# Kernel tuning notes

Measured on AMD Instinct MI355X. Metric: run time of the kernel, lower is better.

The kernel has to match this reference:

```python
import jax, jax.numpy as jnp
import numpy as np

L, ND, ED, AD = 2, 128, 64, 64
N, E, A, G = 50000, 300000, 600000, 16
EPS = 1e-5


def _graph_norm(h, batch, num_graphs, w, b):
    # PyG LayerNorm(mode='graph'): scalar mean/var over all nodes*features per graph.
    F = h.shape[-1]
    cnt = jax.ops.segment_sum(jnp.ones(h.shape[0], h.dtype), batch, num_segments=num_graphs)
    norm = jnp.maximum(cnt, 1.0) * F  # [G]
    mean = (jax.ops.segment_sum(h, batch, num_segments=num_graphs).sum(-1) / norm)[batch][:, None]
    hc = h - mean
    var = (jax.ops.segment_sum(hc * hc, batch, num_segments=num_graphs).sum(-1) / norm)
    out = hc * jax.lax.rsqrt(var + EPS)[batch][:, None]
    return out * w + b


def setup_inputs() -> dict:
    key = jax.random.key(0)
    ks = jax.random.split(key, 24)

    def lin(k, fi, fo):
        return jax.random.normal(k, (L, fi, fo), jnp.float32) / jnp.sqrt(float(fi))

    inp = {
        "x": jax.random.normal(ks[0], (N, ND), jnp.float32),
        "edge_attr": jax.random.normal(ks[1], (E, ED), jnp.float32),
        "angle_attr": jax.random.normal(ks[2], (A, AD), jnp.float32),
        # node_edge_mlp: [2*ND+ED -> ED], plain linear (plain_last=True)
        "W_ne": lin(ks[3], 2 * ND + ED, ED), "b_ne": jnp.zeros((L, ED), jnp.float32),
        "g_e": jnp.ones((L, ED), jnp.float32), "be_e": jnp.zeros((L, ED), jnp.float32),
        # edge_angle_mlp: [2*ED+AD -> AD]
        "W_ea": lin(ks[4], 2 * ED + AD, AD), "b_ea": jnp.zeros((L, AD), jnp.float32),
        "g_a": jnp.ones((L, AD), jnp.float32), "be_a": jnp.zeros((L, AD), jnp.float32),
        # edge_graph_mp message net: [2*ED+AD -> ED]
        "W_emp": lin(ks[5], 2 * ED + AD, ED), "b_emp": jnp.zeros((L, ED), jnp.float32),
        "g_emp": jnp.ones((L, ED), jnp.float32), "be_emp": jnp.zeros((L, ED), jnp.float32),
        # node_graph_mp message net: [2*ND+ED -> ND]
        "W_nmp": lin(ks[6], 2 * ND + ED, ND), "b_nmp": jnp.zeros((L, ND), jnp.float32),
        "g_nmp": jnp.ones((L, ND), jnp.float32), "be_nmp": jnp.zeros((L, ND), jnp.float32),
        "node_batch": jnp.sort(jax.random.randint(ks[7], (N,), 0, G)),
        "edge_index": jax.random.randint(ks[8], (2, E), 0, N),
        "edge_batch": jnp.sort(jax.random.randint(ks[9], (E,), 0, G)),
        "threebody_index": jax.random.randint(ks[10], (2, A), 0, E),
        "angle_batch": jnp.sort(jax.random.randint(ks[11], (A,), 0, G)),
        "num_graphs": G,
    }
    return inp


def reference(x, edge_attr, angle_attr,
              W_ne, b_ne, g_e, be_e,
              W_ea, b_ea, g_a, be_a,
              W_emp, b_emp, g_emp, be_emp,
              W_nmp, b_nmp, g_nmp, be_nmp,
              node_batch, edge_index, edge_batch,
              threebody_index, angle_batch, num_graphs):
    src_e, dst_e = edge_index[0], edge_index[1]
    src_t, dst_t = threebody_index[0], threebody_index[1]
    n_nodes, n_edges = x.shape[0], edge_attr.shape[0]
    for i in range(W_ne.shape[0]):
        # node-pair -> edge update + residual + graph norm
        ecat = jnp.concatenate([x[src_e], x[dst_e], edge_attr], axis=-1)
        edge_attr = edge_attr + ecat @ W_ne[i] + b_ne[i]
        edge_attr = _graph_norm(edge_attr, edge_batch, num_graphs, g_e[i], be_e[i])
        # edge-pair -> angle update + residual + graph norm
        acat = jnp.concatenate([edge_attr[src_t], edge_attr[dst_t], angle_attr], axis=-1)
        angle_attr = angle_attr + acat @ W_ea[i] + b_ea[i]
        angle_attr = _graph_norm(angle_attr, angle_batch, num_graphs, g_a[i], be_a[i])
        # edge_graph_mp: angle-mediated message passing over edges
        mcat = jnp.concatenate([edge_attr[src_t], edge_attr[dst_t], angle_attr], axis=-1)
        msg = jax.nn.relu(mcat @ W_emp[i] + b_emp[i])
        agg = jax.ops.segment_sum(msg, dst_t, num_segments=n_edges)
        edge_attr = _graph_norm(edge_attr + agg, edge_batch, num_graphs, g_emp[i], be_emp[i])
        # node_graph_mp: edge-mediated message passing over nodes
        ncat = jnp.concatenate([x[src_e], x[dst_e], edge_attr], axis=-1)
        nmsg = jax.nn.relu(ncat @ W_nmp[i] + b_nmp[i])
        nagg = jax.ops.segment_sum(nmsg, dst_e, num_segments=n_nodes)
        x = _graph_norm(x + nagg, node_batch, num_graphs, g_nmp[i], be_nmp[i])
    return x
```

## Files before the change

### kernel.cpp

```cpp
#include <hip/hip_runtime.h>

typedef __attribute__((ext_vector_type(8))) short bf16x8_t;
typedef __attribute__((ext_vector_type(4))) short bf16x4_t;
typedef __attribute__((ext_vector_type(4))) float f32x4_t;

constexpr int NG = 16;
constexpr float EPS = 1e-5f;

__device__ inline unsigned short f2bf(float f) {
  unsigned u = __builtin_bit_cast(unsigned, f);
  u += 0x7FFFu + ((u >> 16) & 1u);
  return (unsigned short)(u >> 16);
}
__device__ inline float bf2f(unsigned short u) {
  unsigned x = ((unsigned)u) << 16;
  return __builtin_bit_cast(float, x);
}

template<bool F32>
__device__ inline void ldrow8(const void* base, size_t off, float v[8]) {
  if constexpr (F32) {
    const float* p = (const float*)base + off;
    float4 f0 = *(const float4*)p, f1 = *(const float4*)(p + 4);
    v[0]=f0.x; v[1]=f0.y; v[2]=f0.z; v[3]=f0.w;
    v[4]=f1.x; v[5]=f1.y; v[6]=f1.z; v[7]=f1.w;
  } else {
    bf16x8_t t = *(const bf16x8_t*)((const unsigned short*)base + off);
#pragma unroll
    for (int k = 0; k < 8; ++k) v[k] = bf2f((unsigned short)t[k]);
  }
}

__global__ __launch_bounds__(256) void k_dense_x(
    const float* __restrict__ x,
    const unsigned short* __restrict__ WtNE,
    const unsigned short* __restrict__ WtNM,
    unsigned short* __restrict__ P, int nN)
{
  int gw = (int)((blockIdx.x * 256u + threadIdx.x) >> 6);
  int ntile = nN >> 4;
  if (gw >= ntile) return;
  int lane = threadIdx.x & 63;
  int colb = lane & 15;
  int ko = (lane >> 4) << 3;
  int rowb = (lane >> 4) << 2;
  int row = (gw << 4) + colb;
  const float* xr = x + (size_t)row * 128;
  f32x4_t a1[4] = {}, a2[4] = {}, a3[8] = {}, a4[8] = {};
#pragma unroll
  for (int c = 0; c < 4; ++c) {
    float4 f0 = *(const float4*)(xr + c * 32 + ko);
    float4 f1 = *(const float4*)(xr + c * 32 + ko + 4);
    float vv[8] = {f0.x,f0.y,f0.z,f0.w,f1.x,f1.y,f1.z,f1.w};
    bf16x8_t a;
#pragma unroll
    for (int k = 0; k < 8; ++k) a[k] = (short)f2bf(vv[k]);
#pragma unroll
    for (int nb = 0; nb < 4; ++nb) {
      bf16x8_t b1 = *(const bf16x8_t*)(WtNE + (size_t)(nb * 16 + colb) * 320 + c * 32 + ko);
      a1[nb] = __builtin_amdgcn_mfma_f32_16x16x32_bf16(a, b1, a1[nb], 0, 0, 0);
      bf16x8_t b2 = *(const bf16x8_t*)(WtNE + (size_t)(nb * 16 + colb) * 320 + (c + 4) * 32 + ko);
      a2[nb] = __builtin_amdgcn_mfma_f32_16x16x32_bf16(a, b2, a2[nb], 0, 0, 0);
    }
#pragma unroll
    for (int nb = 0; nb < 8; ++nb) {
      bf16x8_t b3 = *(const bf16x8_t*)(WtNM + (size_t)(nb * 16 + colb) * 320 + c * 32 + ko);
      a3[nb] = __builtin_amdgcn_mfma_f32_16x16x32_bf16(a, b3, a3[nb], 0, 0, 0);
      bf16x8_t b4 = *(const bf16x8_t*)(WtNM + (size_t)(nb * 16 + colb) * 320 + (c + 4) * 32 + ko);
      a4[nb] = __builtin_amdgcn_mfma_f32_16x16x32_bf16(a, b4, a4[nb], 0, 0, 0);
    }
  }
#pragma unroll
  for (int r = 0; r < 4; ++r) {
    size_t ro = (size_t)((gw << 4) + rowb + r) * 384;
    bf16x4_t t1, t2;
#pragma unroll
    for (int nb = 0; nb < 4; ++nb) { t1[nb] = (short)f2bf(a1[nb][r]); t2[nb] = (short)f2bf(a2[nb][r]); }
    *(bf16x4_t*)(P + ro + colb * 4) = t1;
    *(bf16x4_t*)(P + ro + 64 + colb * 4) = t2;
    bf16x8_t t3, t4;
#pragma unroll
    for (int nb = 0; nb < 8; ++nb) { t3[nb] = (short)f2bf(a3[nb][r]); t4[nb] = (short)f2bf(a4[nb][r]); }
    *(bf16x8_t*)(P + ro + 128 + colb * 8) = t3;
    *(bf16x8_t*)(P + ro + 256 + colb * 8) = t4;
  }
}

__global__ __launch_bounds__(256) void k_prep_e(
    const unsigned short* __restrict__ eA, const int* __restrict__ ebatch,
    const float* __restrict__ afA, const float* __restrict__ afB,
    const unsigned short* __restrict__ WtA,
    const unsigned short* __restrict__ WtP,
    unsigned short* __restrict__ PAE, int nE)
{
  __shared__ float lA[1024], lB[1024];
  for (int i = threadIdx.x; i < 1024; i += 256) { lA[i] = afA[i]; lB[i] = afB[i]; }
  __syncthreads();
  int gw = (int)((blockIdx.x * 256u + threadIdx.x) >> 6);
  int ntile = nE >> 4;
  if (gw >= ntile) return;
  int lane = threadIdx.x & 63;
  int colb = lane & 15;
  int ko = (lane >> 4) << 3;
  int rowb = (lane >> 4) << 2;
  int row = (gw << 4) + colb;
  int ge = ebatch[row];
  f32x4_t pa1[4] = {}, pa2[4] = {}, pe3[4] = {}, pe4[4] = {};
#pragma unroll
  for (int c2 = 0; c2 < 2; ++c2) {
    int fb = c2 * 32 + ko;
    bf16x8_t t = *(const bf16x8_t*)(eA + (size_t)row * 64 + fb);
    bf16x8_t an;
#pragma unroll
    for (int k = 0; k < 8; ++k)
      an[k] = (short)f2bf(bf2f((unsigned short)t[k]) * lA[ge*64 + fb + k] + lB[ge*64 + fb + k]);
#pragma unroll
    for (int nb = 0; nb < 4; ++nb) {
      size_t wb = (size_t)(nb * 16 + colb) * 192;
      bf16x8_t b;
      b = *(const bf16x8_t*)(WtA + wb + c2 * 32 + ko);
      pa1[nb] = __builtin_amdgcn_mfma_f32_16x16x32_bf16(an, b, pa1[nb], 0, 0, 0);
      b = *(const bf16x8_t*)(WtA + wb + 64 + c2 * 32 + ko);
      pa2[nb] = __builtin_amdgcn_mfma_f32_16x16x32_bf16(an, b, pa2[nb], 0, 0, 0);
      b = *(const bf16x8_t*)(WtP + wb + c2 * 32 + ko);
      pe3[nb] = __builtin_amdgcn_mfma_f32_16x16x32_bf16(an, b, pe3[nb], 0, 0, 0);
      b = *(const bf16x8_t*)(WtP + wb + 64 + c2 * 32 + ko);
      pe4[nb] = __builtin_amdgcn_mfma_f32_16x16x32_bf16(an, b, pe4[nb], 0, 0, 0);
    }
  }
#pragma unroll
  for (int r = 0; r < 4; ++r) {
    size_t ro = (size_t)((gw << 4) + rowb + r) * 256;
    bf16x8_t sH, dH;
#pragma unroll
    for (int nb = 0; nb < 4; ++nb) {
      sH[nb] = (short)f2bf(pa1[nb][r]); sH[4 + nb] = (short)f2bf(pe3[nb][r]);
      dH[nb] = (short)f2bf(pa2[nb][r]); dH[4 + nb] = (short)f2bf(pe4[nb][r]);
    }
    *(bf16x8_t*)(PAE + ro + colb * 8) = sH;
    *(bf16x8_t*)(PAE + ro + 128 + colb * 8) = dH;
  }
}

template<bool EF32>
__global__ __launch_bounds__(256) void k_edge(
    const unsigned short* __restrict__ P, const void* e_in, unsigned short* e_out,
    const int* __restrict__ ei, const int* __restrict__ ebatch,
    const unsigned short* __restrict__ Wt,
    const float* __restrict__ bias,
    const float* __restrict__ afA, const float* __restrict__ afB,
    float* __restrict__ gs1, float* __restrict__ gs2, int nE)
{
  __shared__ float lA[1024], lB[1024];
  __shared__ float ls1[NG], ls2[NG];
  __shared__ __align__(16) unsigned short tl[4][16][72];
  for (int i = threadIdx.x; i < 1024; i += 256) { lA[i] = afA[i]; lB[i] = afB[i]; }
  if (threadIdx.x < NG) { ls1[threadIdx.x] = 0.f; ls2[threadIdx.x] = 0.f; }
  __syncthreads();
  int gw = (int)((blockIdx.x * 256u + threadIdx.x) >> 6);
  int ntile = nE >> 4;
  bool act = gw < ntile;
  int lane = threadIdx.x & 63;
  int wid = threadIdx.x >> 6;
  int colb = lane & 15;
  int ko = (lane >> 4) << 3;
  int rowb = (lane >> 4) << 2;
  float sr[4] = {0.f,0.f,0.f,0.f}, ssr[4] = {0.f,0.f,0.f,0.f};
  if (act) {
    int sI[4], dI[4];
#pragma unroll
    for (int r = 0; r < 4; ++r) {
      int e_r = (gw << 4) + rowb + r;
      sI[r] = ei[e_r]; dI[r] = ei[nE + e_r];
    }
    bf16x4_t g1[4], g2[4];
#pragma unroll
    for (int r = 0; r < 4; ++r) {
      g1[r] = *(const bf16x4_t*)(P + (size_t)sI[r] * 384 + colb * 4);
      g2[r] = *(const bf16x4_t*)(P + (size_t)dI[r] * 384 + 64 + colb * 4);
    }
    int row = (gw << 4) + colb;
    int ge = ebatch[row];
    f32x4_t acc[4] = {};
#pragma unroll
    for (int c2 = 0; c2 < 2; ++c2) {
      int fb = c2 * 32 + ko;
      float vv[8];
      ldrow8<EF32>(e_in, (size_t)row * 64 + fb, vv);
      bf16x8_t a;
#pragma unroll
      for (int k = 0; k < 8; ++k) a[k] = (short)f2bf(vv[k] * lA[ge*64 + fb + k] + lB[ge*64 + fb + k]);
      *(bf16x8_t*)&tl[wid][colb][fb] = a;
#pragma unroll
      for (int nb = 0; nb < 4; ++nb) {
        bf16x8_t b = *(const bf16x8_t*)(Wt + (size_t)(nb * 16 + colb) * 320 + (8 + c2) * 32 + ko);
        acc[nb] = __builtin_amdgcn_mfma_f32_16x16x32_bf16(a, b, acc[nb], 0, 0, 0);
      }
    }
#pragma unroll
    for (int r = 0; r < 4; ++r) {
      int e_ = (gw << 4) + rowb + r;
#pragma unroll
      for (int nb = 0; nb < 4; ++nb) {
        int col = nb * 16 + colb;
        size_t off = (size_t)e_ * 64 + col;
        float nv = bf2f(tl[wid][rowb + r][col]);
        float vv = nv + bias[col]
                 + acc[nb][r] + bf2f((unsigned short)g1[r][nb]) + bf2f((unsigned short)g2[r][nb]);
        e_out[off] = f2bf(vv);
        sr[r] += vv; ssr[r] += vv * vv;
      }
    }
  }
#pragma unroll
  for (int m = 1; m <= 8; m <<= 1)
#pragma unroll
    for (int r = 0; r < 4; ++r) { sr[r] += __shfl_xor(sr[r], m); ssr[r] += __shfl_xor(ssr[r], m); }
  if (act && colb == 0) {
#pragma unroll
    for (int r = 0; r < 4; ++r) {
      int g = ebatch[(gw << 4) + rowb + r];
      atomicAdd(&ls1[g], sr[r]); atomicAdd(&ls2[g], ssr[r]);
    }
  }
  __syncthreads();
  if (threadIdx.x < NG) {
    atomicAdd(&gs1[threadIdx.x], ls1[threadIdx.x]);
    atomicAdd(&gs2[threadIdx.x], ls2[threadIdx.x]);
  }
}

template<bool AF32>
__global__ __launch_bounds__(256) void k_angle(
    const unsigned short* __restrict__ PAE,
    const void* a_in, unsigned short* a_out,
    const int* __restrict__ ti, const int* __restrict__ abatch,
    const unsigned short* __restrict__ Wt,
    const float* __restrict__ bias,
    const float* __restrict__ afAA, const float* __restrict__ afAB,
    float* __restrict__ gs1, float* __restrict__ gs2,
    unsigned short* __restrict__ pe, int nA)
{
  __shared__ float lAA[1024], lAB[1024];
  __shared__ float ls1[NG], ls2[NG];
  __shared__ __align__(16) unsigned short tl[4][16][72];
  for (int i = threadIdx.x; i < 1024; i += 256) { lAA[i] = afAA[i]; lAB[i] = afAB[i]; }
  if (threadIdx.x < NG) { ls1[threadIdx.x] = 0.f; ls2[threadIdx.x] = 0.f; }
  __syncthreads();
  int gw = (int)((blockIdx.x * 256u + threadIdx.x) >> 6);
  int ntile = nA >> 4;
  bool act = gw < ntile;
  int lane = threadIdx.x & 63;
  int wid = threadIdx.x >> 6;
  int colb = lane & 15;
  int ko = (lane >> 4) << 3;
  int rowb = (lane >> 4) << 2;
  float sr[4] = {0.f,0.f,0.f,0.f}, ssr[4] = {0.f,0.f,0.f,0.f};
  if (act) {
    int sI[4], dI[4];
#pragma unroll
    for (int r = 0; r < 4; ++r) {
      int a_r = (gw << 4) + rowb + r;
      sI[r] = ti[a_r]; dI[r] = ti[nA + a_r];
    }
    bf16x8_t gS[4], gD[4];
#pragma unroll
    for (int r = 0; r < 4; ++r) {
      gS[r] = *(const bf16x8_t*)(PAE + (size_t)sI[r] * 256 + colb * 8);
      gD[r] = *(const bf16x8_t*)(PAE + (size_t)dI[r] * 256 + 128 + colb * 8);
    }
    int row = (gw << 4) + colb;
    int ga = abatch[row];
    f32x4_t acc[4] = {};
#pragma unroll
    for (int c2 = 0; c2 < 2; ++c2) {
      int fb = c2 * 32 + ko;
      float vv[8];
      ldrow8<AF32>(a_in, (size_t)row * 64 + fb, vv);
      bf16x8_t a;
#pragma unroll
      for (int k = 0; k < 8; ++k) a[k] = (short)f2bf(vv[k] * lAA[ga*64 + fb + k] + lAB[ga*64 + fb + k]);
      *(bf16x8_t*)&tl[wid][colb][fb] = a;
#pragma unroll
      for (int nb = 0; nb < 4; ++nb) {
        bf16x8_t b = *(const bf16x8_t*)(Wt + (size_t)(nb * 16 + colb) * 192 + 128 + c2 * 32 + ko);
        acc[nb] = __builtin_amdgcn_mfma_f32_16x16x32_bf16(a, b, acc[nb], 0, 0, 0);
      }
    }
#pragma unroll
    for (int r = 0; r < 4; ++r) {
      int a_ = (gw << 4) + rowb + r;
#pragma unroll
      for (int nb = 0; nb < 4; ++nb) {
        int col = nb * 16 + colb;
        size_t off = (size_t)a_ * 64 + col;
        float nv = bf2f(tl[wid][rowb + r][col]);
        float vv = nv + bias[col] + acc[nb][r]
                 + bf2f((unsigned short)gS[r][nb]) + bf2f((unsigned short)gD[r][nb]);
        a_out[off] = f2bf(vv);
        sr[r] += vv; ssr[r] += vv * vv;
      }
      bf16x4_t pv;
#pragma unroll
      for (int nb = 0; nb < 4; ++nb)
        pv[nb] = (short)f2bf(bf2f((unsigned short)gS[r][4 + nb]) + bf2f((unsigned short)gD[r][4 + nb]));
      *(bf16x4_t*)(pe + (size_t)a_ * 64 + colb * 4) = pv;
    }
  }
#pragma unroll
  for (int m = 1; m <= 8; m <<= 1)
#pragma unroll
    for (int r = 0; r < 4; ++r) { sr[r] += __shfl_xor(sr[r], m); ssr[r] += __shfl_xor(ssr[r], m); }
  if (act && colb == 0) {
#pragma unroll
    for (int r = 0; r < 4; ++r) {
      int g = abatch[(gw << 4) + rowb + r];
      atomicAdd(&ls1[g], sr[r]); atomicAdd(&ls2[g], ssr[r]);
    }
  }
  __syncthreads();
  if (threadIdx.x < NG) {
    atomicAdd(&gs1[threadIdx.x], ls1[threadIdx.x]);
    atomicAdd(&gs2[threadIdx.x], ls2[threadIdx.x]);
  }
}

__global__ __launch_bounds__(256) void k_fin_emp(
    const unsigned short* __restrict__ a_, const int* __restrict__ abatch,
    const unsigned short* __restrict__ Wt,
    const float* __restrict__ bias,
    const float* __restrict__ afAA, const float* __restrict__ afAB,
    unsigned short* __restrict__ msg, int nA)
{
  __shared__ float lAA[1024], lAB[1024];
  for (int i = threadIdx.x; i < 1024; i += 256) { lAA[i] = afAA[i]; lAB[i] = afAB[i]; }
  __syncthreads();
  int gw = (int)((blockIdx.x * 256u + threadIdx.x) >> 6);
  int ntile = nA >> 4;
  if (gw >= ntile) return;
  int lane = threadIdx.x & 63;
  int colb = lane & 15;
  int ko = (lane >> 4) << 3;
  int rowb = (lane >> 4) << 2;
  int row = (gw << 4) + colb;
  int ga = abatch[row];
  f32x4_t acc[4] = {};
#pragma unroll
  for (int c2 = 0; c2 < 2; ++c2) {
    int fb = c2 * 32 + ko;
    bf16x8_t t = *(const bf16x8_t*)(a_ + (size_t)row * 64 + fb);
    bf16x8_t a;
#pragma unroll
    for (int k = 0; k < 8; ++k)
      a[k] = (short)f2bf(bf2f((unsigned short)t[k]) * lAA[ga*64 + fb + k] + lAB[ga*64 + fb + k]);
#pragma unroll
    for (int nb = 0; nb < 4; ++nb) {
      bf16x8_t b = *(const bf16x8_t*)(Wt + (size_t)(nb * 16 + colb) * 192 + 128 + c2 * 32 + ko);
      acc[nb] = __builtin_amdgcn_mfma_f32_16x16x32_bf16(a, b, acc[nb], 0, 0, 0);
    }
  }
  bf16x4_t p4[4];
#pragma unroll
  for (int r = 0; r < 4; ++r)
    p4[r] = *(const bf16x4_t*)(msg + (size_t)((gw << 4) + rowb + r) * 64 + colb * 4);
#pragma unroll
  for (int r = 0; r < 4; ++r) {
    int a_idx = (gw << 4) + rowb + r;
#pragma unroll
    for (int nb = 0; nb < 4; ++nb) {
      int col = nb * 16 + colb;
      float v = fmaxf(acc[nb][r] + bf2f((unsigned short)p4[r][nb]) + bias[col], 0.f);
      msg[(size_t)a_idx * 64 + col] = f2bf(v);
    }
  }
}

__global__ __launch_bounds__(256) void k_fin_nmp(
    const unsigned short* __restrict__ P,
    const unsigned short* __restrict__ e, const int* __restrict__ ei,
    const int* __restrict__ ebatch,
    const unsigned short* __restrict__ Wt,
    const float* __restrict__ bias,
    const float* __restrict__ afEA, const float* __restrict__ afEB,
    unsigned short* __restrict__ msg, int nE)
{
  __shared__ float lEA[1024], lEB[1024];
  for (int i = threadIdx.x; i < 1024; i += 256) { lEA[i] = afEA[i]; lEB[i] = afEB[i]; }
  __syncthreads();
  int gw = (int)((blockIdx.x * 256u + threadIdx.x) >> 6);
  int ntile = nE >> 4;
  if (gw >= ntile) return;
  int lane = threadIdx.x & 63;
  int colb = lane & 15;
  int ko = (lane >> 4) << 3;
  int rowb = (lane >> 4) << 2;
  int sI[4], dI[4];
#pragma unroll
  for (int r = 0; r < 4; ++r) {
    int e_r = (gw << 4) + rowb + r;
    sI[r] = ei[e_r]; dI[r] = ei[nE + e_r];
  }
  bf16x8_t g3[4], g4[4];
#pragma unroll
  for (int r = 0; r < 4; ++r) {
    g3[r] = *(const bf16x8_t*)(P + (size_t)sI[r] * 384 + 128 + colb * 8);
    g4[r] = *(const bf16x8_t*)(P + (size_t)dI[r] * 384 + 256 + colb * 8);
  }
  int row = (gw << 4) + colb;
  int ge = ebatch[row];
  f32x4_t acc[8] = {};
#pragma unroll
  for (int c2 = 0; c2 < 2; ++c2) {
    int fb = c2 * 32 + ko;
    bf16x8_t t = *(const bf16x8_t*)(e + (size_t)row * 64 + fb);
    bf16x8_t a;
#pragma unroll
    for (int k = 0; k < 8; ++k)
      a[k] = (short)f2bf(bf2f((unsigned short)t[k]) * lEA[ge*64 + fb + k] + lEB[ge*64 + fb + k]);
#pragma unroll
    for (int nb = 0; nb < 8; ++nb) {
      bf16x8_t b = *(const bf16x8_t*)(Wt + (size_t)(nb * 16 + colb) * 320 + (8 + c2) * 32 + ko);
      acc[nb] = __builtin_amdgcn_mfma_f32_16x16x32_bf16(a, b, acc[nb], 0, 0, 0);
    }
  }
#pragma unroll
  for (int r = 0; r < 4; ++r) {
    int e_ = (gw << 4) + rowb + r;
#pragma unroll
    for (int nb = 0; nb < 8; ++nb) {
      int col = nb * 16 + colb;
      float v = fmaxf(acc[nb][r] + bf2f((unsigned short)g3[r][nb]) + bf2f((unsigned short)g4[r][nb])
                      + bias[col], 0.f);
      msg[(size_t)e_ * 128 + col] = f2bf(v);
    }
  }
}

__global__ __launch_bounds__(256) void k_red_e(
    const unsigned short* __restrict__ msg, const unsigned short* e_in, unsigned short* e_out,
    const int* __restrict__ ptr, const int* __restrict__ perm,
    const int* __restrict__ ebatch,
    const float* __restrict__ afA, const float* __restrict__ afB,
    float* __restrict__ gs1, float* __restrict__ gs2, int nE)
{
  __shared__ float lA[1024], lB[1024], ls1[NG], ls2[NG];
  for (int i = threadIdx.x; i < 1024; i += 256) { lA[i] = afA[i]; lB[i] = afB[i]; }
  if (threadIdx.x < NG) { ls1[threadIdx.x] = 0.f; ls2[threadIdx.x] = 0.f; }
  __syncthreads();
  int lane = threadIdx.x & 63;
  int wv = (int)((blockIdx.x * 256u + threadIdx.x) >> 6);
  int nw = (int)((gridDim.x * 256u) >> 6);
  for (int eidx = wv; eidx < nE; eidx += nw) {
    int p0 = ptr[eidx], p1 = ptr[eidx + 1];
    float sum = 0.f;
    for (int j = p0; j < p1; ++j) {
      int aidx = perm[j];
      sum += bf2f(msg[(size_t)aidx * 64 + lane]);
    }
    int g = ebatch[eidx];
    size_t off = (size_t)eidx * 64 + lane;
    float v = bf2f(e_in[off]) * lA[g*64 + lane] + lB[g*64 + lane] + sum;
    e_out[off] = f2bf(v);
    float s = v, ss = v * v;
#pragma unroll
    for (int m = 1; m < 64; m <<= 1) { s += __shfl_xor(s, m); ss += __shfl_xor(ss, m); }
    if (lane == 0) { atomicAdd(&ls1[g], s); atomicAdd(&ls2[g], ss); }
  }
  __syncthreads();
  if (threadIdx.x < NG) {
    atomicAdd(&gs1[threadIdx.x], ls1[threadIdx.x]);
    atomicAdd(&gs2[threadIdx.x], ls2[threadIdx.x]);
  }
}

__global__ __launch_bounds__(256) void k_red_n(
    const unsigned short* __restrict__ msg, const float* x_in, float* out,
    const int* __restrict__ ptr, const int* __restrict__ perm,
    const int* __restrict__ nbatch,
    float* __restrict__ gs1, float* __restrict__ gs2, int nN)
{
  __shared__ float ls1[NG], ls2[NG];
  if (threadIdx.x < NG) { ls1[threadIdx.x] = 0.f; ls2[threadIdx.x] = 0.f; }
  __syncthreads();
  int lane = threadIdx.x & 63;
  int wv = (int)((blockIdx.x * 256u + threadIdx.x) >> 6);
  int nw = (int)((gridDim.x * 256u) >> 6);
  for (int n = wv; n < nN; n += nw) {
    int p0 = ptr[n], p1 = ptr[n + 1];
    float s0 = 0.f, s1v = 0.f;
    for (int j = p0; j < p1; ++j) {
      int e = perm[j];
      unsigned u = *(const unsigned*)(msg + (size_t)e * 128 + lane * 2);
      s0 += bf2f((unsigned short)(u & 0xffffu));
      s1v += bf2f((unsigned short)(u >> 16));
    }
    size_t off = (size_t)n * 128 + lane * 2;
    float h0 = x_in[off] + s0, h1 = x_in[off + 1] + s1v;
    out[off] = h0; out[off + 1] = h1;
    float s = h0 + h1, ss = h0 * h0 + h1 * h1;
#pragma unroll
    for (int m = 1; m < 64; m <<= 1) { s += __shfl_xor(s, m); ss += __shfl_xor(ss, m); }
    if (lane == 0) { int g = nbatch[n]; atomicAdd(&ls1[g], s); atomicAdd(&ls2[g], ss); }
  }
  __syncthreads();
  if (threadIdx.x < NG) {
    atomicAdd(&gs1[threadIdx.x], ls1[threadIdx.x]);
    atomicAdd(&gs2[threadIdx.x], ls2[threadIdx.x]);
  }
}

__global__ __launch_bounds__(256) void k_mkaff(
    const float* __restrict__ s1, const float* __restrict__ s2,
    const float* __restrict__ cnt, int F,
    const float* __restrict__ w, const float* __restrict__ b,
    float* __restrict__ A, float* __restrict__ B)
{
  int idx = blockIdx.x * 256 + threadIdx.x;
  if (idx >= NG * F) return;
  int g = idx / F, f = idx - g * F;
  float norm = fmaxf(cnt[g], 1.f) * (float)F;
  float m = s1[g] / norm;
  float var = s2[g] / norm - m * m;
  float inv = rsqrtf(var + EPS);
  float a = inv * w[f];
  A[idx] = a;
  B[idx] = b[f] - m * a;
}

__global__ __launch_bounds__(256) void k_idaff(float* __restrict__ A, float* __restrict__ B, int n)
{
  int idx = blockIdx.x * 256 + threadIdx.x;
  if (idx < n) { A[idx] = 1.f; B[idx] = 0.f; }
}

__global__ __launch_bounds__(256) void k_apply(
    float* h, const int* __restrict__ batch,
    const float* __restrict__ A, const float* __restrict__ B, int nN)
{
  int total = nN * 16;
  int stride = gridDim.x * 256;
  for (int idx = blockIdx.x * 256 + threadIdx.x; idx < total; idx += stride) {
    int row = idx >> 4, q = (idx & 15) * 8;
    int g = batch[row];
    float* hp = h + (size_t)row * 128 + q;
    float4 f0 = *(const float4*)hp;
    float4 f1 = *(const float4*)(hp + 4);
    float vv[8] = {f0.x,f0.y,f0.z,f0.w,f1.x,f1.y,f1.z,f1.w};
#pragma unroll
    for (int k = 0; k < 8; ++k) vv[k] = vv[k] * A[(g << 7) + q + k] + B[(g << 7) + q + k];
    float4 g0 = {vv[0],vv[1],vv[2],vv[3]}, g1 = {vv[4],vv[5],vv[6],vv[7]};
    *(float4*)hp = g0;
    *(float4*)(hp + 4) = g1;
  }
}

__global__ __launch_bounds__(256) void k_count(
    const int* __restrict__ batch, int n, float* __restrict__ cnt)
{
  __shared__ float lc[NG];
  if (threadIdx.x < NG) lc[threadIdx.x] = 0.f;
  __syncthreads();
  for (int i = blockIdx.x * 256 + threadIdx.x; i < n; i += gridDim.x * 256)
    atomicAdd(&lc[batch[i]], 1.f);
  __syncthreads();
  if (threadIdx.x < NG) atomicAdd(&cnt[threadIdx.x], lc[threadIdx.x]);
}

__global__ __launch_bounds__(256) void k_hist(
    const int* __restrict__ dst, int n, int* __restrict__ cnt)
{
  for (int i = blockIdx.x * 256 + threadIdx.x; i < n; i += gridDim.x * 256)
    atomicAdd(&cnt[dst[i]], 1);
}

__global__ __launch_bounds__(256) void k_scan1(
    const int* __restrict__ in, int* __restrict__ out, int* __restrict__ bsum, int n)
{
  __shared__ int wtot[4];
  int tid = threadIdx.x, lane = tid & 63, wid = tid >> 6;
  int base = blockIdx.x * 1024 + tid * 4;
  int v[4];
#pragma unroll
  for (int k = 0; k < 4; ++k) v[k] = (base + k < n) ? in[base + k] : 0;
  int tsum = v[0] + v[1] + v[2] + v[3];
  int incl = tsum;
#pragma unroll
  for (int off = 1; off < 64; off <<= 1) {
    int up = __shfl_up(incl, off);
    if (lane >= off) incl += up;
  }
  if (lane == 63) wtot[wid] = incl;
  __syncthreads();
  if (tid == 0) {
    int r = 0;
#pragma unroll
    for (int w2 = 0; w2 < 4; ++w2) { int t = wtot[w2]; wtot[w2] = r; r += t; }
    bsum[blockIdx.x] = r;
  }
  __syncthreads();
  int excl = wtot[wid] + incl - tsum;
#pragma unroll
  for (int k = 0; k < 4; ++k) {
    if (base + k < n) out[base + k] = excl;
    excl += v[k];
  }
}

__global__ __launch_bounds__(256) void k_scan2(int* __restrict__ bsum, int nb, int* __restrict__ total_out)
{
  __shared__ int wtot[4];
  int tid = threadIdx.x, lane = tid & 63, wid = tid >> 6;
  int base = tid * 4;
  int v[4];
#pragma unroll
  for (int k = 0; k < 4; ++k) v[k] = (base + k < nb) ? bsum[base + k] : 0;
  int tsum = v[0] + v[1] + v[2] + v[3];
  int incl = tsum;
#pragma unroll
  for (int off = 1; off < 64; off <<= 1) {
    int up = __shfl_up(incl, off);
    if (lane >= off) incl += up;
  }
  if (lane == 63) wtot[wid] = incl;
  __syncthreads();
  if (tid == 0) {
    int r = 0;
#pragma unroll
    for (int w2 = 0; w2 < 4; ++w2) { int t = wtot[w2]; wtot[w2] = r; r += t; }
    *total_out = r;
  }
  __syncthreads();
  int excl = wtot[wid] + incl - tsum;
#pragma unroll
  for (int k = 0; k < 4; ++k) {
    if (base + k < nb) bsum[base + k] = excl;
    excl += v[k];
  }
}

__global__ __launch_bounds__(256) void k_scan3(
    int* __restrict__ ptr, int* __restrict__ cur, const int* __restrict__ bsum, int n)
{
  for (int i = blockIdx.x * 256 + threadIdx.x; i < n; i += gridDim.x * 256) {
    int v = ptr[i] + bsum[i >> 10];
    ptr[i] = v; cur[i] = v;
  }
}

__global__ __launch_bounds__(256) void k_scatter(
    const int* __restrict__ dst, int* __restrict__ cur, int* __restrict__ perm, int n)
{
  for (int i = blockIdx.x * 256 + threadIdx.x; i < n; i += gridDim.x * 256) {
    int d = dst[i];
    int p = atomicAdd(&cur[d], 1);
    perm[p] = i;
  }
}

__global__ __launch_bounds__(256) void k_wt(
    const float* __restrict__ W, unsigned short* __restrict__ Wt, int K, int NO)
{
  int idx = blockIdx.x * 256 + threadIdx.x;
  if (idx >= K * NO) return;
  int k = idx / NO, j = idx - k * NO;
  Wt[(size_t)j * K + k] = f2bf(W[idx]);
}

extern "C" void kernel_launch(void* const* d_in, const int* in_sizes, int n_in,
                              void* d_out, int out_size, void* d_ws, size_t ws_size,
                              hipStream_t stream)
{
  const float* x0    = (const float*)d_in[0];
  const float* e0    = (const float*)d_in[1];
  const float* a0    = (const float*)d_in[2];
  const float* W_ne  = (const float*)d_in[3];
  const float* b_ne  = (const float*)d_in[4];
  const float* g_e   = (const float*)d_in[5];
  const float* be_e  = (const float*)d_in[6];
  const float* W_ea  = (const float*)d_in[7];
  const float* b_ea  = (const float*)d_in[8];
  const float* g_a   = (const float*)d_in[9];
  const float* be_a  = (const float*)d_in[10];
  const float* W_emp = (const float*)d_in[11];
  const float* b_emp = (const float*)d_in[12];
  const float* g_emp = (const float*)d_in[13];
  const float* be_emp= (const float*)d_in[14];
  const float* W_nmp = (const float*)d_in[15];
  const float* b_nmp = (const float*)d_in[16];
  const float* g_nmp = (const float*)d_in[17];
  const float* be_nmp= (const float*)d_in[18];
  const int* node_batch  = (const int*)d_in[19];
  const int* edge_index  = (const int*)d_in[20];
  const int* edge_batch  = (const int*)d_in[21];
  const int* tb_index    = (const int*)d_in[22];
  const int* angle_batch = (const int*)d_in[23];

  const int N = in_sizes[0] / 128;
  const int E = in_sizes[1] / 64;
  const int A = in_sizes[2] / 64;

  char* wsp = (char*)d_ws;
  auto alloc = [&](size_t bytes) { char* p = wsp; wsp += (bytes + 255) & ~(size_t)255; return p; };
  unsigned short* eAB  = (unsigned short*)alloc((size_t)E * 64 * 2);
  unsigned short* aAB  = (unsigned short*)alloc((size_t)A * 64 * 2);
  unsigned short* msg  = (unsigned short*)alloc((size_t)A * 64 * 2);
  unsigned short* P    = (unsigned short*)alloc((size_t)N * 384 * 2);
  unsigned short* PAE  = (unsigned short*)alloc((size_t)E * 256 * 2);
  int* ptr_n  = (int*)alloc((size_t)(N + 1) * 4);
  int* cur_n  = (int*)alloc((size_t)N * 4);
  int* perm_n = (int*)alloc((size_t)E * 4);
  int* ptr_e  = (int*)alloc((size_t)(E + 1) * 4);
  int* cur_e  = (int*)alloc((size_t)E * 4);
  int* perm_e = (int*)alloc((size_t)A * 4);
  int* bsum   = (int*)alloc(4096 * 4);
  float* stats = (float*)alloc(5 * NG * 4);
  float* s1    = stats;
  float* s2    = stats + NG;
  float* cnt_n = stats + 2 * NG;
  float* cnt_e = stats + 3 * NG;
  float* cnt_a = stats + 4 * NG;
  float* afE_idA = (float*)alloc(1024 * 4); float* afE_idB = (float*)alloc(1024 * 4);
  float* afA_idA = (float*)alloc(1024 * 4); float* afA_idB = (float*)alloc(1024 * 4);
  float* afE1A   = (float*)alloc(1024 * 4); float* afE1B   = (float*)alloc(1024 * 4);
  float* afE2A   = (float*)alloc(1024 * 4); float* afE2B   = (float*)alloc(1024 * 4);
  float* afA1A   = (float*)alloc(1024 * 4); float* afA1B   = (float*)alloc(1024 * 4);
  float* afXA    = (float*)alloc(2048 * 4); float* afXB    = (float*)alloc(2048 * 4);
  unsigned short* wt_ne  = (unsigned short*)alloc((size_t)2 * 320 * 64 * 2);
  unsigned short* wt_ea  = (unsigned short*)alloc((size_t)2 * 192 * 64 * 2);
  unsigned short* wt_emp = (unsigned short*)alloc((size_t)2 * 192 * 64 * 2);
  unsigned short* wt_nmp = (unsigned short*)alloc((size_t)2 * 320 * 128 * 2);

  float* x_out = (float*)d_out;

  for (int i = 0; i < 2; ++i) {
    k_wt<<<(320*64 + 255)/256, 256, 0, stream>>>(W_ne  + (size_t)i*320*64,  wt_ne  + (size_t)i*320*64,  320, 64);
    k_wt<<<(192*64 + 255)/256, 256, 0, stream>>>(W_ea  + (size_t)i*192*64,  wt_ea  + (size_t)i*192*64,  192, 64);
    k_wt<<<(192*64 + 255)/256, 256, 0, stream>>>(W_emp + (size_t)i*192*64,  wt_emp + (size_t)i*192*64,  192, 64);
    k_wt<<<(320*128 + 255)/256, 256, 0, stream>>>(W_nmp + (size_t)i*320*128, wt_nmp + (size_t)i*320*128, 320, 128);
  }
  hipMemsetAsync(stats, 0, 5 * NG * 4, stream);
  k_count<<<512, 256, 0, stream>>>(node_batch, N, cnt_n);
  k_count<<<512, 256, 0, stream>>>(edge_batch, E, cnt_e);
  k_count<<<512, 256, 0, stream>>>(angle_batch, A, cnt_a);
  k_idaff<<<4, 256, 0, stream>>>(afE_idA, afE_idB, 1024);
  k_idaff<<<4, 256, 0, stream>>>(afA_idA, afA_idB, 1024);

  hipMemsetAsync(cur_n, 0, (size_t)N * 4, stream);
  hipMemsetAsync(cur_e, 0, (size_t)E * 4, stream);
  k_hist<<<1024, 256, 0, stream>>>(edge_index + E, E, cur_n);
  k_hist<<<1024, 256, 0, stream>>>(tb_index + A, A, cur_e);
  int nbN = (N + 1023) / 1024, nbE = (E + 1023) / 1024;
  k_scan1<<<nbN, 256, 0, stream>>>(cur_n, ptr_n, bsum, N);
  k_scan2<<<1, 256, 0, stream>>>(bsum, nbN, ptr_n + N);
  k_scan3<<<1024, 256, 0, stream>>>(ptr_n, cur_n, bsum, N);
  k_scatter<<<1024, 256, 0, stream>>>(edge_index + E, cur_n, perm_n, E);
  k_scan1<<<nbE, 256, 0, stream>>>(cur_e, ptr_e, bsum, E);
  k_scan2<<<1, 256, 0, stream>>>(bsum, nbE, ptr_e + E);
  k_scan3<<<1024, 256, 0, stream>>>(ptr_e, cur_e, bsum, E);
  k_scatter<<<1024, 256, 0, stream>>>(tb_index + A, cur_e, perm_e, A);

  const float* x_cur = x0;
  int blkE = (E / 16 + 3) / 4;
  int blkA = (A / 16 + 3) / 4;
  int blkN = (N / 16 + 3) / 4;

  for (int i = 0; i < 2; ++i) {
    const float* fEinA = (i == 0) ? afE_idA : afE2A;
    const float* fEinB = (i == 0) ? afE_idB : afE2B;
    const float* fAinA = (i == 0) ? afA_idA : afA1A;
    const float* fAinB = (i == 0) ? afA_idB : afA1B;

    k_dense_x<<<blkN, 256, 0, stream>>>(x_cur, wt_ne + (size_t)i*320*64,
                                        wt_nmp + (size_t)i*320*128, P, N);

    hipMemsetAsync(s1, 0, 2 * NG * 4, stream);
    if (i == 0)
      k_edge<true><<<blkE, 256, 0, stream>>>(P, (const void*)e0, eAB, edge_index, edge_batch,
                                             wt_ne + (size_t)i*320*64, b_ne + i*64,
                                             fEinA, fEinB, s1, s2, E);
    else
      k_edge<false><<<blkE, 256, 0, stream>>>(P, (const void*)eAB, eAB, edge_index, edge_batch,
                                              wt_ne + (size_t)i*320*64, b_ne + i*64,
                                              fEinA, fEinB, s1, s2, E);
    k_mkaff<<<4, 256, 0, stream>>>(s1, s2, cnt_e, 64, g_e + i*64, be_e + i*64, afE1A, afE1B);

    k_prep_e<<<blkE, 256, 0, stream>>>(eAB, edge_batch, afE1A, afE1B,
                                       wt_ea + (size_t)i*192*64, wt_emp + (size_t)i*192*64,
                                       PAE, E);

    hipMemsetAsync(s1, 0, 2 * NG * 4, stream);
    if (i == 0)
      k_angle<true><<<blkA, 256, 0, stream>>>(PAE, (const void*)a0, aAB, tb_index, angle_batch,
                                              wt_ea + (size_t)i*192*64, b_ea + i*64,
                                              fAinA, fAinB, s1, s2, msg, A);
    else
      k_angle<false><<<blkA, 256, 0, stream>>>(PAE, (const void*)aAB, aAB, tb_index, angle_batch,
                                               wt_ea + (size_t)i*192*64, b_ea + i*64,
                                               fAinA, fAinB, s1, s2, msg, A);
    k_mkaff<<<4, 256, 0, stream>>>(s1, s2, cnt_a, 64, g_a + i*64, be_a + i*64, afA1A, afA1B);

    k_fin_emp<<<blkA, 256, 0, stream>>>(aAB, angle_batch, wt_emp + (size_t)i*192*64,
                                        b_emp + i*64, afA1A, afA1B, msg, A);
    hipMemsetAsync(s1, 0, 2 * NG * 4, stream);
    k_red_e<<<2048, 256, 0, stream>>>(msg, eAB, eAB, ptr_e, perm_e, edge_batch,
                                      afE1A, afE1B, s1, s2, E);
    k_mkaff<<<4, 256, 0, stream>>>(s1, s2, cnt_e, 64, g_emp + i*64, be_emp + i*64, afE2A, afE2B);

    k_fin_nmp<<<blkE, 256, 0, stream>>>(P, eAB, edge_index, edge_batch,
                                        wt_nmp + (size_t)i*320*128, b_nmp + i*128,
                                        afE2A, afE2B, msg, E);
    hipMemsetAsync(s1, 0, 2 * NG * 4, stream);
    k_red_n<<<2048, 256, 0, stream>>>(msg, x_cur, x_out, ptr_n, perm_n, node_batch,
                                      s1, s2, N);
    k_mkaff<<<8, 256, 0, stream>>>(s1, s2, cnt_n, 128, g_nmp + i*128, be_nmp + i*128, afXA, afXB);
    k_apply<<<2048, 256, 0, stream>>>(x_out, node_batch, afXA, afXB, N);

    x_cur = x_out;
  }
}
```

Before: 1.615 ms.

## Gather emp edge projections directly in fin_emp instead of staging partial sums

The PAE layout is reordered so the angle-update and message-net projections for each edge endpoint sit in separate 64-wide chunks. k_angle now gathers only the 8-byte angle-update half and no longer writes the precomputed src+dst message partial to the msg buffer. k_fin_emp instead re-reads the triplet indices and gathers the message-net halves itself. This removes one 600K×64 bf16 write and read of intermediate data, at the cost of a second index load and a second random gather in k_fin_emp.

Measured after the change: 1.628 ms. Within noise of the previous version (+0.8%).

```diff
diff --git a/kernel.cpp b/kernel.cpp
--- a/kernel.cpp
+++ b/kernel.cpp
@@ -131,14 +131,16 @@
 #pragma unroll
   for (int r = 0; r < 4; ++r) {
     size_t ro = (size_t)((gw << 4) + rowb + r) * 256;
-    bf16x8_t sH, dH;
+    bf16x4_t t1, t3, t2, t4;
 #pragma unroll
     for (int nb = 0; nb < 4; ++nb) {
-      sH[nb] = (short)f2bf(pa1[nb][r]); sH[4 + nb] = (short)f2bf(pe3[nb][r]);
-      dH[nb] = (short)f2bf(pa2[nb][r]); dH[4 + nb] = (short)f2bf(pe4[nb][r]);
-    }
-    *(bf16x8_t*)(PAE + ro + colb * 8) = sH;
-    *(bf16x8_t*)(PAE + ro + 128 + colb * 8) = dH;
+      t1[nb] = (short)f2bf(pa1[nb][r]); t3[nb] = (short)f2bf(pe3[nb][r]);
+      t2[nb] = (short)f2bf(pa2[nb][r]); t4[nb] = (short)f2bf(pe4[nb][r]);
+    }
+    *(bf16x4_t*)(PAE + ro + colb * 4) = t1;
+    *(bf16x4_t*)(PAE + ro + 64 + colb * 4) = t3;
+    *(bf16x4_t*)(PAE + ro + 128 + colb * 4) = t2;
+    *(bf16x4_t*)(PAE + ro + 192 + colb * 4) = t4;
   }
 }
 
@@ -238,8 +240,7 @@
     const unsigned short* __restrict__ Wt,
     const float* __restrict__ bias,
     const float* __restrict__ afAA, const float* __restrict__ afAB,
-    float* __restrict__ gs1, float* __restrict__ gs2,
-    unsigned short* __restrict__ pe, int nA)
+    float* __restrict__ gs1, float* __restrict__ gs2, int nA)
 {
   __shared__ float lAA[1024], lAB[1024];
   __shared__ float ls1[NG], ls2[NG];
@@ -263,11 +264,11 @@
       int a_r = (gw << 4) + rowb + r;
       sI[r] = ti[a_r]; dI[r] = ti[nA + a_r];
     }
-    bf16x8_t gS[4], gD[4];
+    bf16x4_t gS[4], gD[4];
 #pragma unroll
     for (int r = 0; r < 4; ++r) {
-      gS[r] = *(const bf16x8_t*)(PAE + (size_t)sI[r] * 256 + colb * 8);
-      gD[r] = *(const bf16x8_t*)(PAE + (size_t)dI[r] * 256 + 128 + colb * 8);
+      gS[r] = *(const bf16x4_t*)(PAE + (size_t)sI[r] * 256 + colb * 4);
+      gD[r] = *(const bf16x4_t*)(PAE + (size_t)dI[r] * 256 + 128 + colb * 4);
     }
     int row = (gw << 4) + colb;
     int ga = abatch[row];
@@ -300,11 +301,6 @@
         a_out[off] = f2bf(vv);
         sr[r] += vv; ssr[r] += vv * vv;
       }
-      bf16x4_t pv;
-#pragma unroll
-      for (int nb = 0; nb < 4; ++nb)
-        pv[nb] = (short)f2bf(bf2f((unsigned short)gS[r][4 + nb]) + bf2f((unsigned short)gD[r][4 + nb]));
-      *(bf16x4_t*)(pe + (size_t)a_ * 64 + colb * 4) = pv;
     }
   }
 #pragma unroll
@@ -326,7 +322,9 @@
 }
 
 __global__ __launch_bounds__(256) void k_fin_emp(
-    const unsigned short* __restrict__ a_, const int* __restrict__ abatch,
+    const unsigned short* __restrict__ PAE,
+    const unsigned short* __restrict__ a_, const int* __restrict__ ti,
+    const int* __restrict__ abatch,
     const unsigned short* __restrict__ Wt,
     const float* __restrict__ bias,
     const float* __restrict__ afAA, const float* __restrict__ afAB,
@@ -342,6 +340,18 @@
   int colb = lane & 15;
   int ko = (lane >> 4) << 3;
   int rowb = (lane >> 4) << 2;
+  int sI[4], dI[4];
+#pragma unroll
+  for (int r = 0; r < 4; ++r) {
+    int a_r = (gw << 4) + rowb + r;
+    sI[r] = ti[a_r]; dI[r] = ti[nA + a_r];
+  }
+  bf16x4_t g3[4], g4[4];
+#pragma unroll
+  for (int r = 0; r < 4; ++r) {
+    g3[r] = *(const bf16x4_t*)(PAE + (size_t)sI[r] * 256 + 64 + colb * 4);
+    g4[r] = *(const bf16x4_t*)(PAE + (size_t)dI[r] * 256 + 192 + colb * 4);
+  }
   int row = (gw << 4) + colb;
   int ga = abatch[row];
   f32x4_t acc[4] = {};
@@ -359,17 +369,14 @@
       acc[nb] = __builtin_amdgcn_mfma_f32_16x16x32_bf16(a, b, acc[nb], 0, 0, 0);
     }
   }
-  bf16x4_t p4[4];
-#pragma unroll
-  for (int r = 0; r < 4; ++r)
-    p4[r] = *(const bf16x4_t*)(msg + (size_t)((gw << 4) + rowb + r) * 64 + colb * 4);
 #pragma unroll
   for (int r = 0; r < 4; ++r) {
     int a_idx = (gw << 4) + rowb + r;
 #pragma unroll
     for (int nb = 0; nb < 4; ++nb) {
       int col = nb * 16 + colb;
-      float v = fmaxf(acc[nb][r] + bf2f((unsigned short)p4[r][nb]) + bias[col], 0.f);
+      float v = fmaxf(acc[nb][r] + bf2f((unsigned short)g3[r][nb]) + bf2f((unsigned short)g4[r][nb])
+                      + bias[col], 0.f);
       msg[(size_t)a_idx * 64 + col] = f2bf(v);
     }
   }
@@ -792,15 +799,16 @@
     if (i == 0)
       k_angle<true><<<blkA, 256, 0, stream>>>(PAE, (const void*)a0, aAB, tb_index, angle_batch,
                                               wt_ea + (size_t)i*192*64, b_ea + i*64,
-                                              fAinA, fAinB, s1, s2, msg, A);
+                                              fAinA, fAinB, s1, s2, A);
     else
       k_angle<false><<<blkA, 256, 0, stream>>>(PAE, (const void*)aAB, aAB, tb_index, angle_batch,
                                                wt_ea + (size_t)i*192*64, b_ea + i*64,
-                                               fAinA, fAinB, s1, s2, msg, A);
+                                               fAinA, fAinB, s1, s2, A);
     k_mkaff<<<4, 256, 0, stream>>>(s1, s2, cnt_a, 64, g_a + i*64, be_a + i*64, afA1A, afA1B);
 
-    k_fin_emp<<<blkA, 256, 0, stream>>>(aAB, angle_batch, wt_emp + (size_t)i*192*64,
-                                        b_emp + i*64, afA1A, afA1B, msg, A);
+    k_fin_emp<<<blkA, 256, 0, stream>>>(PAE, aAB, tb_index, angle_batch,
+                                        wt_emp + (size_t)i*192*64, b_emp + i*64,
+                                        afA1A, afA1B, msg, A);
     hipMemsetAsync(s1, 0, 2 * NG * 4, stream);
     k_red_e<<<2048, 256, 0, stream>>>(msg, eAB, eAB, ptr_e, perm_e, edge_batch,
                                       afE1A, afE1B, s1, s2, E);
```
